# Kernel optimization log

Hardware: AMD Instinct MI355X
Metric: run time of the kernel (lower is better)

## Reference

```python
import jax, jax.numpy as jnp
import numpy as np

B = 2048
GIN = 128      # gating input features
GH = 128       # gating hidden units
E = 8          # experts
XIN = 512      # expert input features
U = 512        # expert layer units
OUT = 512      # expert output features


def setup_inputs() -> dict:
    key = jax.random.key(0)
    ks = jax.random.split(key, 16)
    rn = lambda k, shape: (jax.random.normal(k, shape) * 0.05).astype(jnp.float32)
    return {
        "gating_input": jax.random.normal(ks[0], (B, GIN), dtype=jnp.float32),
        "expert_input": jax.random.normal(ks[1], (B, XIN), dtype=jnp.float32),
        # gating MLP params (Dense stores kernel as (in, out))
        "Wg0": rn(ks[2], (GIN, GH)), "bg0": rn(ks[3], (GH,)),
        "Wg1": rn(ks[4], (GH, GH)), "bg1": rn(ks[5], (GH,)),
        "Wgo": rn(ks[6], (GH, E)),  "bgo": rn(ks[7], (E,)),
        # expert weight pools: alpha (E, units, in), beta (E, units)
        "alpha0": rn(ks[8], (E, U, XIN)), "beta0": rn(ks[9], (E, U)),
        "alpha1": rn(ks[10], (E, U, U)),  "beta1": rn(ks[11], (E, U)),
        "alpha2": rn(ks[12], (E, OUT, U)), "beta2": rn(ks[13], (E, OUT)),
    }


def dense_expert(x, g, alpha, beta):
    # Mathematically: (sum_e g[b,e] * alpha[e]) @ x[b] + sum_e g[b,e]*beta[e]
    # Contract input with each expert first (avoids the (B,U,I) blended-weight tensor).
    per_expert = jnp.einsum("bi,eui->beu", x, alpha)   # (B, E, U)
    w = jnp.einsum("be,beu->bu", g, per_expert)         # (B, U)
    b = jnp.einsum("be,eu->bu", g, beta)                # (B, U)
    return w + b


def reference(gating_input, expert_input, Wg0, bg0, Wg1, bg1, Wgo, bgo,
              alpha0, beta0, alpha1, beta1, alpha2, beta2):
    # Gating network: Dense+ELU x2 (dropout is identity at inference), Dense+softmax
    h = jax.nn.elu(gating_input @ Wg0 + bg0)
    h = jax.nn.elu(h @ Wg1 + bg1)
    g = jax.nn.softmax(h @ Wgo + bgo, axis=-1)          # (B, E)

    # Expert network: DenseExpert + ELU x2, final DenseExpert
    x = jax.nn.elu(dense_expert(expert_input, g, alpha0, beta0))
    x = jax.nn.elu(dense_expert(x, g, alpha1, beta1))
    y = dense_expert(x, g, alpha2, beta2)               # (B, OUT)
    return y
```

## Files before the change

### kernel.cpp

```cpp
#include <hip/hip_runtime.h>
#include <math.h>

#define BATCH 2048
#define GIN 128
#define GH 128
#define NE 8
#define XIN 512
#define UU 512

typedef __attribute__((ext_vector_type(8))) short short8;
typedef __attribute__((ext_vector_type(4))) float f32x4;

#define AS1 __attribute__((address_space(1)))
#define AS3 __attribute__((address_space(3)))

__device__ inline unsigned short f2bf(float f) {
    unsigned u = __float_as_uint(f);
    u += 0x7fffu + ((u >> 16) & 1u);
    return (unsigned short)(u >> 16);
}

__device__ inline float elu1(float x) { return x > 0.f ? x : (expf(x) - 1.f); }

__global__ __launch_bounds__(256) void gating_kernel(
    const float* __restrict__ gin, const float* __restrict__ W0, const float* __restrict__ b0,
    const float* __restrict__ W1, const float* __restrict__ b1,
    const float* __restrict__ Wo, const float* __restrict__ bo,
    float* __restrict__ g)
{
    __shared__ float xs[4][128];
    __shared__ float hs[4][128];
    __shared__ float ps[2][4][128];
    __shared__ float lp[8][4][8];
    __shared__ float ls[4][8];

    const int t = threadIdx.x;
    const int c = t & 127;
    const int h = t >> 7;
    const int row0 = blockIdx.x * 4;

    ((float*)xs)[t]       = gin[row0 * GIN + t];
    ((float*)xs)[t + 256] = gin[row0 * GIN + t + 256];
    __syncthreads();

    {
        float acc0 = 0.f, acc1 = 0.f, acc2 = 0.f, acc3 = 0.f;
        const float* Wc = W0 + c;
        #pragma unroll 8
        for (int i = h * 64; i < h * 64 + 64; ++i) {
            float w = Wc[i * GH];
            acc0 += xs[0][i] * w; acc1 += xs[1][i] * w;
            acc2 += xs[2][i] * w; acc3 += xs[3][i] * w;
        }
        ps[h][0][c] = acc0; ps[h][1][c] = acc1; ps[h][2][c] = acc2; ps[h][3][c] = acc3;
    }
    __syncthreads();
    {
        int o = t, r = o >> 7, cc = o & 127;
        hs[r][cc] = elu1(ps[0][r][cc] + ps[1][r][cc] + b0[cc]);
        o = t + 256; r = o >> 7; cc = o & 127;
        hs[r][cc] = elu1(ps[0][r][cc] + ps[1][r][cc] + b0[cc]);
    }
    __syncthreads();

    {
        float acc0 = 0.f, acc1 = 0.f, acc2 = 0.f, acc3 = 0.f;
        const float* Wc = W1 + c;
        #pragma unroll 8
        for (int i = h * 64; i < h * 64 + 64; ++i) {
            float w = Wc[i * GH];
            acc0 += hs[0][i] * w; acc1 += hs[1][i] * w;
            acc2 += hs[2][i] * w; acc3 += hs[3][i] * w;
        }
        ps[h][0][c] = acc0; ps[h][1][c] = acc1; ps[h][2][c] = acc2; ps[h][3][c] = acc3;
    }
    __syncthreads();
    {
        int o = t, r = o >> 7, cc = o & 127;
        xs[r][cc] = elu1(ps[0][r][cc] + ps[1][r][cc] + b1[cc]);
        o = t + 256; r = o >> 7; cc = o & 127;
        xs[r][cc] = elu1(ps[0][r][cc] + ps[1][r][cc] + b1[cc]);
    }
    __syncthreads();

    {
        const int e = t & 7, r = (t >> 3) & 3, q = t >> 5;
        float s = 0.f;
        #pragma unroll
        for (int i = q * 16; i < q * 16 + 16; ++i) s += xs[r][i] * Wo[i * NE + e];
        lp[q][r][e] = s;
    }
    __syncthreads();
    if (t < 32) {
        const int r = t >> 3, e = t & 7;
        float s = bo[e];
        #pragma unroll
        for (int q = 0; q < 8; ++q) s += lp[q][r][e];
        ls[r][e] = s;
    }
    __syncthreads();
    if (t < 4) {
        float mx = ls[t][0];
        #pragma unroll
        for (int e = 1; e < 8; ++e) mx = fmaxf(mx, ls[t][e]);
        float s = 0.f, ex[8];
        #pragma unroll
        for (int e = 0; e < 8; ++e) { ex[e] = expf(ls[t][e] - mx); s += ex[e]; }
        float inv = 1.f / s;
        #pragma unroll
        for (int e = 0; e < 8; ++e) g[(row0 + t) * NE + e] = ex[e] * inv;
    }
}

__global__ __launch_bounds__(256) void convert_kernel(
    const float* __restrict__ a0, const float* __restrict__ a1, const float* __restrict__ a2,
    const float* __restrict__ xv, unsigned short* __restrict__ dst)
{
    const long long vi = (long long)(blockIdx.x * blockDim.x + threadIdx.x) * 4;
    const int sel = (int)(vi >> 21);
    const float* src = (sel == 0) ? a0 : (sel == 1) ? a1 : (sel == 2) ? a2 : xv;
    float4 v = *(const float4*)(src + (vi & ((1 << 21) - 1)));
    union { unsigned short us[4]; uint2 u2; } p;
    p.us[0] = f2bf(v.x); p.us[1] = f2bf(v.y); p.us[2] = f2bf(v.z); p.us[3] = f2bf(v.w);
    *(uint2*)(dst + vi) = p.u2;
}

__global__ __launch_bounds__(256) void moe_fused_kernel(
    const unsigned short* __restrict__ A,
    const unsigned short* __restrict__ Bw,
    const float* __restrict__ g,
    const float* __restrict__ beta,
    unsigned short* __restrict__ Xnext,
    float* __restrict__ out, int last)
{
    constexpr int K = XIN;
    __shared__ unsigned short As[2][64 * 32];
    __shared__ unsigned short Bs[2][8 * 32 * 32];
    __shared__ float gs[64][8];
    __shared__ float bt[8][32];

    const int t = threadIdx.x;
    const int n0 = blockIdx.x * 32;
    const int m0 = blockIdx.y * 64;
    const int wave = t >> 6, lane = t & 63;
    const int e0 = 2 * wave;

    ((float2*)gs)[t] = ((const float2*)(g + (size_t)m0 * NE))[t];
    bt[t >> 5][t & 31] = beta[(t >> 5) * UU + n0 + (t & 31)];

    f32x4 acc[2][4][2] = {};

    const int slot = t & 3;
    const int arow = t >> 2;
    const int acol = ((slot ^ ((arow >> 1) & 3)) * 8);
    const unsigned short* a_src = A + (size_t)(m0 + arow) * K + acol;

    const unsigned short* b_src[4];
    #pragma unroll
    for (int it = 0; it < 4; ++it) {
        const int rowflat = it * 64 + arow;
        const int bcol = ((slot ^ ((rowflat >> 1) & 3)) * 8);
        b_src[it] = Bw + ((size_t)(rowflat >> 5) * UU + n0 + (rowflat & 31)) * K + bcol;
    }

#define STAGE(bi, ki)                                                        \
    do {                                                                     \
        __builtin_amdgcn_global_load_lds(                                    \
            (const AS1 void*)(a_src + (ki)),                                 \
            (AS3 void*)(&As[bi][t * 8]), 16, 0, 0);                          \
        _Pragma("unroll")                                                    \
        for (int it_ = 0; it_ < 4; ++it_)                                    \
            __builtin_amdgcn_global_load_lds(                                \
                (const AS1 void*)(b_src[it_] + (ki)),                        \
                (AS3 void*)(&Bs[bi][it_ * 2048 + t * 8]), 16, 0, 0);         \
    } while (0)

#define COMPUTE(bi)                                                          \
    do {                                                                     \
        const int fr_ = lane & 15;                                           \
        const int fkb_ = (lane >> 4) * 16;                                   \
        short8 af_[4], bf_[2][2];                                            \
        _Pragma("unroll")                                                    \
        for (int i = 0; i < 4; ++i) {                                        \
            const int row_ = fr_ + i * 16;                                   \
            af_[i] = *(const short8*)((const char*)(&As[bi][0]) +            \
                     ((row_ * 64 + fkb_) ^ (((row_ >> 1) & 3) << 4)));       \
        }                                                                    \
        _Pragma("unroll")                                                    \
        for (int ep = 0; ep < 2; ++ep)                                       \
            _Pragma("unroll")                                                \
            for (int j = 0; j < 2; ++j) {                                    \
                const int row_ = (e0 + ep) * 32 + j * 16 + fr_;              \
                bf_[ep][j] = *(const short8*)((const char*)(&Bs[bi][0]) +    \
                     ((row_ * 64 + fkb_) ^ (((row_ >> 1) & 3) << 4)));       \
            }                                                                \
        _Pragma("unroll")                                                    \
        for (int ep = 0; ep < 2; ++ep)                                       \
            _Pragma("unroll")                                                \
            for (int i = 0; i < 4; ++i)                                      \
                _Pragma("unroll")                                            \
                for (int j = 0; j < 2; ++j)                                  \
                    acc[ep][i][j] = __builtin_amdgcn_mfma_f32_16x16x32_bf16( \
                        af_[i], bf_[ep][j], acc[ep][i][j], 0, 0, 0);         \
    } while (0)

    STAGE(0, 0);
    __syncthreads();

    for (int step = 0; step < 15; ++step) {
        const int cur = step & 1;
        STAGE(cur ^ 1, (step + 1) * 32);
        COMPUTE(cur);
        __syncthreads();
    }
    COMPUTE(1);

    __syncthreads();
    float* red = (float*)&Bs[0][0];

    const int cl = lane & 15, rq = lane >> 4;
    #pragma unroll
    for (int i = 0; i < 4; ++i)
        #pragma unroll
        for (int j = 0; j < 2; ++j)
            #pragma unroll
            for (int r = 0; r < 4; ++r) {
                const int rl = i * 16 + rq * 4 + r;
                const int co = j * 16 + cl;
                const float v =
                    gs[rl][e0]     * (acc[0][i][j][r] + bt[e0][co]) +
                    gs[rl][e0 + 1] * (acc[1][i][j][r] + bt[e0 + 1][co]);
                red[wave * 2048 + rl * 32 + co] = v;
            }
    __syncthreads();

    {
        const int rl = t >> 2;
        const int c0 = (t & 3) * 8;
        float v[8];
        #pragma unroll
        for (int u = 0; u < 8; ++u) {
            const int idx = rl * 32 + c0 + u;
            v[u] = red[idx] + red[2048 + idx] + red[4096 + idx] + red[6144 + idx];
        }
        if (last) {
            float4 o0 = {v[0], v[1], v[2], v[3]};
            float4 o1 = {v[4], v[5], v[6], v[7]};
            float* op = out + (size_t)(m0 + rl) * UU + n0 + c0;
            *(float4*)op = o0;
            *(float4*)(op + 4) = o1;
        } else {
            union { unsigned short us[8]; short8 s8; } p;
            #pragma unroll
            for (int u = 0; u < 8; ++u) p.us[u] = f2bf(elu1(v[u]));
            *(short8*)(Xnext + (size_t)(m0 + rl) * UU + n0 + c0) = p.s8;
        }
    }
#undef STAGE
#undef COMPUTE
}

extern "C" void kernel_launch(void* const* d_in, const int* in_sizes, int n_in,
                              void* d_out, int out_size, void* d_ws, size_t ws_size,
                              hipStream_t stream)
{
    (void)in_sizes; (void)n_in; (void)out_size; (void)ws_size;
    const float* gin = (const float*)d_in[0];
    const float* xin = (const float*)d_in[1];
    const float* W0  = (const float*)d_in[2];
    const float* b0  = (const float*)d_in[3];
    const float* W1  = (const float*)d_in[4];
    const float* b1  = (const float*)d_in[5];
    const float* Wo  = (const float*)d_in[6];
    const float* bo  = (const float*)d_in[7];
    const float* alpha[3] = {(const float*)d_in[8],  (const float*)d_in[10], (const float*)d_in[12]};
    const float* beta[3]  = {(const float*)d_in[9],  (const float*)d_in[11], (const float*)d_in[13]};
    float* out = (float*)d_out;

    char* ws = (char*)d_ws;
    float* g = (float*)ws;
    size_t off = 65536;
    unsigned short* ab = (unsigned short*)(ws + off);
    off += (size_t)3 * (1 << 21) * 2;
    unsigned short* Xb0 = (unsigned short*)(ws + off);
    off += (size_t)BATCH * XIN * 2;
    unsigned short* Xb1 = (unsigned short*)(ws + off);
    off += (size_t)BATCH * XIN * 2;

    gating_kernel<<<BATCH / 4, 256, 0, stream>>>(gin, W0, b0, W1, b1, Wo, bo, g);
    convert_kernel<<<(3 * (1 << 21) + BATCH * XIN) / 4 / 256, 256, 0, stream>>>(
        alpha[0], alpha[1], alpha[2], xin, ab);

    unsigned short* Xsrc = Xb0;
    unsigned short* Xdst = Xb1;
    for (int l = 0; l < 3; ++l) {
        moe_fused_kernel<<<dim3(UU / 32, BATCH / 64), 256, 0, stream>>>(
            Xsrc, ab + (size_t)l * (1 << 21), g, beta[l], Xdst, out, l == 2 ? 1 : 0);
        unsigned short* tmp = Xsrc; Xsrc = Xdst; Xdst = tmp;
    }
}
```

Baseline: 153.2 us.

## Load expert weights directly into registers and merge gating with conversion

```diff
diff --git a/kernel.cpp b/kernel.cpp
--- a/kernel.cpp
+++ b/kernel.cpp
@@ -22,11 +22,13 @@
 
 __device__ inline float elu1(float x) { return x > 0.f ? x : (expf(x) - 1.f); }
 
-__global__ __launch_bounds__(256) void gating_kernel(
+__global__ __launch_bounds__(256) void pre_kernel(
     const float* __restrict__ gin, const float* __restrict__ W0, const float* __restrict__ b0,
     const float* __restrict__ W1, const float* __restrict__ b1,
     const float* __restrict__ Wo, const float* __restrict__ bo,
-    float* __restrict__ g)
+    float* __restrict__ g,
+    const float* __restrict__ a0, const float* __restrict__ a1, const float* __restrict__ a2,
+    const float* __restrict__ xv, unsigned short* __restrict__ dst)
 {
     __shared__ float xs[4][128];
     __shared__ float hs[4][128];
@@ -35,6 +37,18 @@
     __shared__ float ls[4][8];
 
     const int t = threadIdx.x;
+
+    if (blockIdx.x >= 512) {
+        const long long vi = ((long long)(blockIdx.x - 512) * 256 + t) * 4;
+        const int sel = (int)(vi >> 21);
+        const float* src = (sel == 0) ? a0 : (sel == 1) ? a1 : (sel == 2) ? a2 : xv;
+        float4 v = *(const float4*)(src + (vi & ((1 << 21) - 1)));
+        union { unsigned short us[4]; uint2 u2; } p;
+        p.us[0] = f2bf(v.x); p.us[1] = f2bf(v.y); p.us[2] = f2bf(v.z); p.us[3] = f2bf(v.w);
+        *(uint2*)(dst + vi) = p.u2;
+        return;
+    }
+
     const int c = t & 127;
     const int h = t >> 7;
     const int row0 = blockIdx.x * 4;
@@ -112,20 +126,7 @@
     }
 }
 
-__global__ __launch_bounds__(256) void convert_kernel(
-    const float* __restrict__ a0, const float* __restrict__ a1, const float* __restrict__ a2,
-    const float* __restrict__ xv, unsigned short* __restrict__ dst)
-{
-    const long long vi = (long long)(blockIdx.x * blockDim.x + threadIdx.x) * 4;
-    const int sel = (int)(vi >> 21);
-    const float* src = (sel == 0) ? a0 : (sel == 1) ? a1 : (sel == 2) ? a2 : xv;
-    float4 v = *(const float4*)(src + (vi & ((1 << 21) - 1)));
-    union { unsigned short us[4]; uint2 u2; } p;
-    p.us[0] = f2bf(v.x); p.us[1] = f2bf(v.y); p.us[2] = f2bf(v.z); p.us[3] = f2bf(v.w);
-    *(uint2*)(dst + vi) = p.u2;
-}
-
-__global__ __launch_bounds__(256) void moe_fused_kernel(
+__global__ __launch_bounds__(256) void moe_layer_kernel(
     const unsigned short* __restrict__ A,
     const unsigned short* __restrict__ Bw,
     const float* __restrict__ g,
@@ -135,13 +136,14 @@
 {
     constexpr int K = XIN;
     __shared__ unsigned short As[2][64 * 32];
-    __shared__ unsigned short Bs[2][8 * 32 * 32];
+    __shared__ float red[4][64][32];
     __shared__ float gs[64][8];
     __shared__ float bt[8][32];
 
     const int t = threadIdx.x;
-    const int n0 = blockIdx.x * 32;
-    const int m0 = blockIdx.y * 64;
+    const int bid = blockIdx.x;
+    const int n0 = (bid & 15) * 32;
+    const int m0 = (bid >> 4) * 64;
     const int wave = t >> 6, lane = t & 63;
     const int e0 = 2 * wave;
 
@@ -155,45 +157,39 @@
     const int acol = ((slot ^ ((arow >> 1) & 3)) * 8);
     const unsigned short* a_src = A + (size_t)(m0 + arow) * K + acol;
 
-    const unsigned short* b_src[4];
+    const int fr = lane & 15;
+    const int kq = (lane >> 4) * 8;
+    const unsigned short* b_ptr[2][2];
     #pragma unroll
-    for (int it = 0; it < 4; ++it) {
-        const int rowflat = it * 64 + arow;
-        const int bcol = ((slot ^ ((rowflat >> 1) & 3)) * 8);
-        b_src[it] = Bw + ((size_t)(rowflat >> 5) * UU + n0 + (rowflat & 31)) * K + bcol;
-    }
-
-#define STAGE(bi, ki)                                                        \
+    for (int ep = 0; ep < 2; ++ep)
+        #pragma unroll
+        for (int j = 0; j < 2; ++j)
+            b_ptr[ep][j] = Bw + ((size_t)(e0 + ep) * UU + n0 + j * 16 + fr) * K + kq;
+
+#define STAGE_A(bi, ki)                                                      \
+    __builtin_amdgcn_global_load_lds(                                        \
+        (const AS1 void*)(a_src + (ki)),                                     \
+        (AS3 void*)(&As[bi][t * 8]), 16, 0, 0)
+
+#define LOADB(dst, ki)                                                       \
     do {                                                                     \
-        __builtin_amdgcn_global_load_lds(                                    \
-            (const AS1 void*)(a_src + (ki)),                                 \
-            (AS3 void*)(&As[bi][t * 8]), 16, 0, 0);                          \
-        _Pragma("unroll")                                                    \
-        for (int it_ = 0; it_ < 4; ++it_)                                    \
-            __builtin_amdgcn_global_load_lds(                                \
-                (const AS1 void*)(b_src[it_] + (ki)),                        \
-                (AS3 void*)(&Bs[bi][it_ * 2048 + t * 8]), 16, 0, 0);         \
+        dst[0] = *(const short8*)(b_ptr[0][0] + (ki));                       \
+        dst[1] = *(const short8*)(b_ptr[0][1] + (ki));                       \
+        dst[2] = *(const short8*)(b_ptr[1][0] + (ki));                       \
+        dst[3] = *(const short8*)(b_ptr[1][1] + (ki));                       \
     } while (0)
 
-#define COMPUTE(bi)                                                          \
+#define COMPUTE(bi, bf)                                                      \
     do {                                                                     \
-        const int fr_ = lane & 15;                                           \
         const int fkb_ = (lane >> 4) * 16;                                   \
-        short8 af_[4], bf_[2][2];                                            \
+        const char* Ab_ = (const char*)(&As[bi][0]);                         \
+        short8 af_[4];                                                       \
         _Pragma("unroll")                                                    \
         for (int i = 0; i < 4; ++i) {                                        \
-            const int row_ = fr_ + i * 16;                                   \
-            af_[i] = *(const short8*)((const char*)(&As[bi][0]) +            \
+            const int row_ = fr + i * 16;                                    \
+            af_[i] = *(const short8*)(Ab_ +                                  \
                      ((row_ * 64 + fkb_) ^ (((row_ >> 1) & 3) << 4)));       \
         }                                                                    \
-        _Pragma("unroll")                                                    \
-        for (int ep = 0; ep < 2; ++ep)                                       \
-            _Pragma("unroll")                                                \
-            for (int j = 0; j < 2; ++j) {                                    \
-                const int row_ = (e0 + ep) * 32 + j * 16 + fr_;              \
-                bf_[ep][j] = *(const short8*)((const char*)(&Bs[bi][0]) +    \
-                     ((row_ * 64 + fkb_) ^ (((row_ >> 1) & 3) << 4)));       \
-            }                                                                \
         _Pragma("unroll")                                                    \
         for (int ep = 0; ep < 2; ++ep)                                       \
             _Pragma("unroll")                                                \
@@ -201,22 +197,26 @@
                 _Pragma("unroll")                                            \
                 for (int j = 0; j < 2; ++j)                                  \
                     acc[ep][i][j] = __builtin_amdgcn_mfma_f32_16x16x32_bf16( \
-                        af_[i], bf_[ep][j], acc[ep][i][j], 0, 0, 0);         \
+                        af_[i], bf[ep * 2 + j], acc[ep][i][j], 0, 0, 0);     \
     } while (0)
 
-    STAGE(0, 0);
-    __syncthreads();
-
-    for (int step = 0; step < 15; ++step) {
-        const int cur = step & 1;
-        STAGE(cur ^ 1, (step + 1) * 32);
-        COMPUTE(cur);
+    short8 bb0[4], bb1[4];
+
+    STAGE_A(0, 0);
+    LOADB(bb0, 0);
+    __syncthreads();
+
+    #pragma unroll
+    for (int s = 0; s < 16; ++s) {
+        if (s < 15) {
+            STAGE_A((s + 1) & 1, (s + 1) * 32);
+            if (s & 1) LOADB(bb0, (s + 1) * 32);
+            else       LOADB(bb1, (s + 1) * 32);
+        }
+        if (s & 1) COMPUTE(1, bb1);
+        else       COMPUTE(0, bb0);
         __syncthreads();
     }
-    COMPUTE(1);
-
-    __syncthreads();
-    float* red = (float*)&Bs[0][0];
 
     const int cl = lane & 15, rq = lane >> 4;
     #pragma unroll
@@ -230,7 +230,7 @@
                 const float v =
                     gs[rl][e0]     * (acc[0][i][j][r] + bt[e0][co]) +
                     gs[rl][e0 + 1] * (acc[1][i][j][r] + bt[e0 + 1][co]);
-                red[wave * 2048 + rl * 32 + co] = v;
+                red[wave][rl][co] = v;
             }
     __syncthreads();
 
@@ -239,10 +239,9 @@
         const int c0 = (t & 3) * 8;
         float v[8];
         #pragma unroll
-        for (int u = 0; u < 8; ++u) {
-            const int idx = rl * 32 + c0 + u;
-            v[u] = red[idx] + red[2048 + idx] + red[4096 + idx] + red[6144 + idx];
-        }
+        for (int u = 0; u < 8; ++u)
+            v[u] = red[0][rl][c0 + u] + red[1][rl][c0 + u] +
+                   red[2][rl][c0 + u] + red[3][rl][c0 + u];
         if (last) {
             float4 o0 = {v[0], v[1], v[2], v[3]};
             float4 o1 = {v[4], v[5], v[6], v[7]};
@@ -256,7 +255,8 @@
             *(short8*)(Xnext + (size_t)(m0 + rl) * UU + n0 + c0) = p.s8;
         }
     }
-#undef STAGE
+#undef STAGE_A
+#undef LOADB
 #undef COMPUTE
 }
 
@@ -287,14 +287,14 @@
     unsigned short* Xb1 = (unsigned short*)(ws + off);
     off += (size_t)BATCH * XIN * 2;
 
-    gating_kernel<<<BATCH / 4, 256, 0, stream>>>(gin, W0, b0, W1, b1, Wo, bo, g);
-    convert_kernel<<<(3 * (1 << 21) + BATCH * XIN) / 4 / 256, 256, 0, stream>>>(
+    pre_kernel<<<512 + 7168, 256, 0, stream>>>(
+        gin, W0, b0, W1, b1, Wo, bo, g,
         alpha[0], alpha[1], alpha[2], xin, ab);
 
     unsigned short* Xsrc = Xb0;
     unsigned short* Xdst = Xb1;
     for (int l = 0; l < 3; ++l) {
-        moe_fused_kernel<<<dim3(UU / 32, BATCH / 64), 256, 0, stream>>>(
+        moe_layer_kernel<<<512, 256, 0, stream>>>(
             Xsrc, ab + (size_t)l * (1 << 21), g, beta[l], Xdst, out, l == 2 ? 1 : 0);
         unsigned short* tmp = Xsrc; Xsrc = Xdst; Xdst = tmp;
     }
```

Result: slower. 162.6 us (+6.1%).
